# Kernel optimization log

Hardware: AMD Instinct MI355X
Metric: run time of the kernel (lower is better)

The kernel has to match this reference:

```python
import jax, jax.numpy as jnp
import numpy as np

MAX_RADIUS = 3.0
N_BASIS = 3
H = 100
C_IN = 23
N_ATOMS = 286
B = 32
Y0 = 1.0 / (2.0 * np.sqrt(np.pi))  # l=0 spherical harmonic


def cosine_basis(r):
    # e3nn CosineBasisModel basis: triangle-clamped then cosine bump
    radii = jnp.linspace(0.0, MAX_RADIUS, N_BASIS)
    step = radii[1] - radii[0]
    z = (r[..., None] - radii) / step                      # [..., N_BASIS]
    tri = 1.0 - jax.nn.relu(2.0 - jax.nn.relu(z + 1.0))    # clamp to [-1, 1]
    return jnp.cos(0.5 * jnp.pi * tri)


def setup_inputs() -> dict:
    key = jax.random.key(0)
    ks = jax.random.split(key, 10)
    def lin(k, fan_in, fan_out):
        return jax.random.normal(k, (fan_in, fan_out), jnp.float32) / np.sqrt(fan_in)
    return {
        "x": jax.random.normal(ks[0], (B, 1), jnp.float32),
        "features": jax.random.normal(ks[1], (B, N_ATOMS, C_IN), jnp.float32),
        "geometry": jax.random.normal(ks[2], (B, N_ATOMS, 3), jnp.float32),
        # radial MLP (CosineBasisModel, L=1 hidden layer of width h=100)
        "rW1": lin(ks[3], N_BASIS, H), "rb1": jnp.zeros((H,), jnp.float32),
        "rW2": lin(ks[4], H, C_IN),    "rb2": jnp.zeros((C_IN,), jnp.float32),
        # MLP head
        "fc1W": lin(ks[5], N_ATOMS, 30), "fc1b": jnp.zeros((30,), jnp.float32),
        "fc2W": lin(ks[6], 30, 10),      "fc2b": jnp.zeros((10,), jnp.float32),
        "fc3W": lin(ks[7], 10, 1),       "fc3b": jnp.zeros((1,), jnp.float32),
    }


def reference(x, features, geometry, rW1, rb1, rW2, rb2,
              fc1W, fc1b, fc2W, fc2b, fc3W, fc3b):
    Bz, N, _ = features.shape
    # pairwise distances r_ab = |geom_b - geom_a|, [B, N, N]
    diff = geometry[:, None, :, :] - geometry[:, :, None, :]
    r = jnp.sqrt(jnp.sum(diff * diff, axis=-1) + 1e-12)
    # radial kernel: cosine basis -> MLP -> 23 scalar-path weights per pair
    basis = cosine_basis(r)                                  # [B, N, N, 3]
    h = jax.nn.relu(basis @ rW1 + rb1)                       # [B, N, N, 100]
    R = (h @ rW2 + rb2) * Y0                                 # [B, N, N, 23]
    # scalar (l=0 -> l=0) point convolution, normalized by 1/sqrt(N)
    feats_new = jnp.einsum('zabj,zbj->za', R, features) * (1.0 / np.sqrt(N))
    # MLP head (fc1 consumes the [B, 286] conv output directly)
    out = jax.nn.relu(feats_new @ fc1W + fc1b)
    out = jax.nn.relu(out @ fc2W + fc2b)
    return out @ fc3W + fc3b                                 # [B, 1]
```

## Files before the change

### kernel.cpp

```cpp
#include <hip/hip_runtime.h>

#define NA      286
#define CIN     23
#define NKH     100
#define NKP     50
#define KPH     25
#define BATCH   32
#define NB_PAD  320
#define TB      64
#define ATILE   12
#define APW     3
#define NTILE_A 24
#define NTILE_B 5
#define KQ_N    5
#define KQ_SZ   10

#define Y0F      0.28209479177387814f
#define RSQRT_N  0.05913123960994873f

typedef _Float16 h2v __attribute__((ext_vector_type(2)));
union F4H { float4 f; h2v h[4]; };

__device__ __forceinline__ h2v h2_splat(float x) {
    _Float16 v = (_Float16)x;
    h2v r; r.x = v; r.y = v; return r;
}
__device__ __forceinline__ h2v h2_pack(float a, float b) {
    h2v r; r.x = (_Float16)a; r.y = (_Float16)b; return r;
}
__device__ __forceinline__ h2v h2_fma(h2v a, h2v b, h2v c) {
#if __has_builtin(__builtin_elementwise_fma)
    return __builtin_elementwise_fma(a, b, c);
#else
    return a * b + c;
#endif
}
__device__ __forceinline__ h2v h2_max0(h2v a) {
    h2v z; z.x = (_Float16)0.f; z.y = (_Float16)0.f;
#if __has_builtin(__builtin_elementwise_max)
    return __builtin_elementwise_max(a, z);
#else
    h2v r; r.x = a.x > z.x ? a.x : z.x; r.y = a.y > z.y ? a.y : z.y; return r;
#endif
}
__device__ __forceinline__ float fdot2f(h2v a, h2v b, float c) {
#if __has_builtin(__builtin_amdgcn_fdot2)
    return __builtin_amdgcn_fdot2(a, b, c, false);
#else
    return c + (float)a.x * (float)b.x + (float)a.y * (float)b.y;
#endif
}

__device__ __forceinline__ float cos_half_pi(float x) {
    float t = 1.5707963267948966f * x;
    float w = t * t;
    return 1.f + w * (-0.5f + w * (4.16666667e-2f + w * (-1.38888889e-3f
               + w * 2.48015873e-5f)));
}

__global__ void __launch_bounds__(256) prep_kernel(
    const float* __restrict__ feat,
    const float* __restrict__ rW2,
    const float* __restrict__ rW1,
    const float* __restrict__ rb1,
    h2v* __restrict__ cbuf2,
    float4* __restrict__ wpk)
{
    __shared__ float flds[TB * CIN];
    __shared__ float wlds[2 * KQ_SZ * CIN];
    const int tid = threadIdx.x;
    const int bT  = blockIdx.x;
    const int z   = blockIdx.y;
    const int kQ  = blockIdx.z;

    if (bT == 0 && z == 0 && kQ == 0 && tid < NKP) {
        int k0 = 2 * tid, k1 = k0 + 1;
        F4H u;
        u.h[0] = h2_pack(rW1[k0],           rW1[k1]);
        u.h[1] = h2_pack(rW1[NKH + k0],     rW1[NKH + k1]);
        u.h[2] = h2_pack(rW1[2 * NKH + k0], rW1[2 * NKH + k1]);
        u.h[3] = h2_pack(rb1[k0],           rb1[k1]);
        wpk[tid] = u.f;
    }

    const int b0 = bT * TB;
    const int nf = ((NA - b0 < TB) ? (NA - b0) : TB) * CIN;
    const float* fsrc = feat + ((size_t)z * NA + b0) * CIN;
    for (int i = tid; i < TB * CIN; i += 256)
        flds[i] = (i < nf) ? fsrc[i] : 0.f;
    const float* wsrc = rW2 + (size_t)kQ * KQ_SZ * 2 * CIN;
    for (int i = tid; i < 2 * KQ_SZ * CIN; i += 256)
        wlds[i] = wsrc[i];
    __syncthreads();

    for (int i = tid; i < TB * KQ_SZ; i += 256) {
        int b   = i & 63;
        int kpl = i >> 6;
        const float* w0 = &wlds[(2 * kpl) * CIN];
        const float* w1 = &wlds[(2 * kpl + 1) * CIN];
        const float* fb = &flds[b * CIN];
        float s0 = 0.f, s1 = 0.f;
#pragma unroll
        for (int j = 0; j < CIN; ++j) {
            s0 = fmaf(fb[j], w0[j], s0);
            s1 = fmaf(fb[j], w1[j], s1);
        }
        int kp = kQ * KQ_SZ + kpl;
        cbuf2[((size_t)z * NKP + kp) * NB_PAD + b0 + b] = h2_pack(s0 * Y0F, s1 * Y0F);
    }
}

__global__ void __launch_bounds__(256) pair_kernel(
    const float* __restrict__ geom,
    const h2v* __restrict__ cbuf2,
    const float4* __restrict__ wpk,
    float* __restrict__ feats_part)
{
    __shared__ float ga[ATILE * 3];

    const int tid   = threadIdx.x;
    const int z     = blockIdx.y;
    const int kh    = blockIdx.z;
    const int aBase = blockIdx.x * ATILE;

    if (tid < ATILE * 3) {
        int aa = aBase + tid / 3;
        int d  = tid - 3 * (tid / 3);
        ga[tid] = (aa < NA) ? geom[((size_t)z * NA + aa) * 3 + d] : 0.f;
    }
    __syncthreads();

    const int wave = tid >> 6;
    const int lane = tid & 63;

    float acc[APW] = {0.f, 0.f, 0.f};
    const h2v*    csrc = cbuf2 + ((size_t)z * NKP + kh * KPH) * NB_PAD;
    const float4* wsrc = wpk + kh * KPH;

    for (int t = 0; t < NTILE_B; ++t) {
        const int b = t * TB + lane;
        float gbx = 0.f, gby = 0.f, gbz = 0.f;
        if (b < NA) {
            const float* g = geom + ((size_t)z * NA + b) * 3;
            gbx = g[0]; gby = g[1]; gbz = g[2];
        }

        h2v u0[APW], u1[APW], u2[APW];
#pragma unroll
        for (int i = 0; i < APW; ++i) {
            const float* gp = &ga[(wave * APW + i) * 3];
            float dx = gbx - gp[0], dy = gby - gp[1], dz = gbz - gp[2];
            float r  = sqrtf(fmaf(dx, dx, fmaf(dy, dy, fmaf(dz, dz, 1e-12f))));
            float zz = r * (1.f / 1.5f);
            u0[i] = h2_splat(cos_half_pi(fminf(zz, 1.f)));
            u1[i] = h2_splat(cos_half_pi(fminf(fmaxf(zz - 1.f, -1.f), 1.f)));
            u2[i] = h2_splat(cos_half_pi(fminf(fmaxf(zz - 2.f, -1.f), 1.f)));
        }

        const h2v* cp = csrc + t * TB + lane;
#pragma unroll 5
        for (int kp = 0; kp < KPH; ++kp) {
            F4H u; u.f = wsrc[kp];
            h2v cb = cp[(size_t)kp * NB_PAD];
#pragma unroll
            for (int i = 0; i < APW; ++i) {
                h2v s = h2_fma(u0[i], u.h[0],
                        h2_fma(u1[i], u.h[1],
                        h2_fma(u2[i], u.h[2], u.h[3])));
                acc[i] = fdot2f(h2_max0(s), cb, acc[i]);
            }
        }
    }

#pragma unroll
    for (int i = 0; i < APW; ++i) {
        float v = acc[i];
        for (int off = 32; off; off >>= 1) v += __shfl_xor(v, off);
        if (lane == 0) {
            int a = aBase + wave * APW + i;
            if (a < NA) feats_part[((size_t)kh * BATCH + z) * 288 + a] = v * RSQRT_N;
        }
    }
}

__global__ void __launch_bounds__(256) head_kernel(
    const float* __restrict__ featsP,
    const float* __restrict__ featIn,
    const float* __restrict__ rb2,
    const float* __restrict__ fc1W, const float* __restrict__ fc1b,
    const float* __restrict__ fc2W, const float* __restrict__ fc2b,
    const float* __restrict__ fc3W, const float* __restrict__ fc3b,
    float* __restrict__ out)
{
    __shared__ float fsum[NA];
    __shared__ float ps[8][CIN];
    __shared__ float po[8][30], pw[8][30];
    __shared__ float czs;
    __shared__ float h1[30], hh2[10];

    const int z = blockIdx.x, tid = threadIdx.x;

    for (int a = tid; a < NA; a += 256)
        fsum[a] = featsP[z * 288 + a] + featsP[(BATCH + z) * 288 + a];

    if (tid < 8 * CIN) {
        int j = tid % CIN, ch = tid / CIN;
        int b0 = ch * 36, b1 = (b0 + 36 < NA) ? b0 + 36 : NA;
        float s = 0.f;
        for (int b = b0; b < b1; ++b) s += featIn[((size_t)z * NA + b) * CIN + j];
        ps[ch][j] = s;
    }
    __syncthreads();
    if (tid < CIN) {
        float s = 0.f;
#pragma unroll
        for (int ch = 0; ch < 8; ++ch) s += ps[ch][tid];
        ps[0][tid] = s * rb2[tid];
    }
    __syncthreads();
    if (tid == 0) {
        float s = 0.f;
#pragma unroll
        for (int j = 0; j < CIN; ++j) s += ps[0][j];
        czs = s * (Y0F * RSQRT_N);
    }

    if (tid < 240) {
        int j = tid % 30, ch = tid / 30;
        int a0 = ch * 36, a1 = (a0 + 36 < NA) ? a0 + 36 : NA;
        float o = 0.f, ws = 0.f;
        for (int a = a0; a < a1; ++a) {
            float w = fc1W[a * 30 + j];
            o  = fmaf(fsum[a], w, o);
            ws += w;
        }
        po[ch][j] = o; pw[ch][j] = ws;
    }
    __syncthreads();
    if (tid < 30) {
        float o = 0.f, ws = 0.f;
#pragma unroll
        for (int ch = 0; ch < 8; ++ch) { o += po[ch][tid]; ws += pw[ch][tid]; }
        h1[tid] = fmaxf(o + czs * ws + fc1b[tid], 0.f);
    }
    __syncthreads();
    if (tid < 10) {
        float v = fc2b[tid];
#pragma unroll
        for (int t = 0; t < 30; ++t) v = fmaf(h1[t], fc2W[t * 10 + tid], v);
        hh2[tid] = fmaxf(v, 0.f);
    }
    __syncthreads();
    if (tid == 0) {
        float v = fc3b[0];
#pragma unroll
        for (int t = 0; t < 10; ++t) v = fmaf(hh2[t], fc3W[t], v);
        out[z] = v;
    }
}

extern "C" void kernel_launch(void* const* d_in, const int* in_sizes, int n_in,
                              void* d_out, int out_size, void* d_ws, size_t ws_size,
                              hipStream_t stream) {
    const float* features = (const float*)d_in[1];
    const float* geometry = (const float*)d_in[2];
    const float* rW1  = (const float*)d_in[3];
    const float* rb1  = (const float*)d_in[4];
    const float* rW2  = (const float*)d_in[5];
    const float* rb2  = (const float*)d_in[6];
    const float* fc1W = (const float*)d_in[7];
    const float* fc1b = (const float*)d_in[8];
    const float* fc2W = (const float*)d_in[9];
    const float* fc2b = (const float*)d_in[10];
    const float* fc3W = (const float*)d_in[11];
    const float* fc3b = (const float*)d_in[12];

    char* ws = (char*)d_ws;
    float4* wpk    = (float4*)ws;
    h2v*    cbuf2  = (h2v*)(ws + 1024);
    float*  featsP = (float*)(ws + 1024 + (size_t)BATCH * NKP * NB_PAD * 4);

    float* out = (float*)d_out;

    prep_kernel<<<dim3(NTILE_B, BATCH, KQ_N), 256, 0, stream>>>(
        features, rW2, rW1, rb1, cbuf2, wpk);
    pair_kernel<<<dim3(NTILE_A, BATCH, 2), 256, 0, stream>>>(
        geometry, cbuf2, wpk, featsP);
    head_kernel<<<BATCH, 256, 0, stream>>>(
        featsP, features, rb2, fc1W, fc1b, fc2W, fc2b, fc3W, fc3b, out);
}
```

Baseline: 143.4 us.

## Split pair kernel over b-tiles, stage c-buffer and weights in LDS

The pair kernel's grid dimension changes from two halves of the hidden units to five b-atom tiles. Each block loads its 50x64 c-buffer slice and the packed radial weights into LDS, and computes the cosine basis once per block rather than once per tile loop iteration. The head kernel now sums five partial outputs instead of two, and a few loops get unroll pragmas. This adds parallelism and replaces global/L2 loads in the inner loop with LDS reads, at the cost of more LDS traffic and a larger partial-output buffer.

```diff
diff --git a/kernel.cpp b/kernel.cpp
--- a/kernel.cpp
+++ b/kernel.cpp
@@ -4,7 +4,6 @@
 #define CIN     23
 #define NKH     100
 #define NKP     50
-#define KPH     25
 #define BATCH   32
 #define NB_PAD  320
 #define TB      64
@@ -110,65 +109,79 @@
     }
 }
 
-__global__ void __launch_bounds__(256) pair_kernel(
+__global__ void __launch_bounds__(256, 8) pair_kernel(
     const float* __restrict__ geom,
     const h2v* __restrict__ cbuf2,
     const float4* __restrict__ wpk,
     float* __restrict__ feats_part)
 {
-    __shared__ float ga[ATILE * 3];
+    __shared__ h2v    c_lds[NKP * TB];
+    __shared__ float4 w_lds[NKP];
+    __shared__ float  ga[ATILE * 3];
 
     const int tid   = threadIdx.x;
     const int z     = blockIdx.y;
-    const int kh    = blockIdx.z;
+    const int bT    = blockIdx.z;
     const int aBase = blockIdx.x * ATILE;
 
-    if (tid < ATILE * 3) {
-        int aa = aBase + tid / 3;
-        int d  = tid - 3 * (tid / 3);
-        ga[tid] = (aa < NA) ? geom[((size_t)z * NA + aa) * 3 + d] : 0.f;
+    {
+        const uint4* s4 = (const uint4*)(cbuf2 + (size_t)z * NKP * NB_PAD + bT * TB);
+        uint4*       d4 = (uint4*)c_lds;
+#pragma unroll
+        for (int r = 0; r < 4; ++r) {
+            int i = r * 256 + tid;
+            if (i < NKP * 16) {
+                int row = i >> 4, col = i & 15;
+                d4[i] = s4[(size_t)row * (NB_PAD / 4) + col];
+            }
+        }
+    }
+    if (tid < NKP) ((uint4*)w_lds)[tid] = ((const uint4*)wpk)[tid];
+    if (tid >= 128 && tid < 128 + ATILE * 3) {
+        int t  = tid - 128;
+        int aa = aBase + t / 3;
+        int d  = t - 3 * (t / 3);
+        ga[t] = (aa < NA) ? geom[((size_t)z * NA + aa) * 3 + d] : 0.f;
     }
     __syncthreads();
 
     const int wave = tid >> 6;
     const int lane = tid & 63;
 
+    const int b = bT * TB + lane;
+    float gbx = 0.f, gby = 0.f, gbz = 0.f;
+    if (b < NA) {
+        const float* g = geom + ((size_t)z * NA + b) * 3;
+        gbx = g[0]; gby = g[1]; gbz = g[2];
+    }
+
+    h2v u0[APW], u1[APW], u2[APW];
+#pragma unroll
+    for (int i = 0; i < APW; ++i) {
+        float axv = ga[(wave * APW + i) * 3 + 0];
+        float ayv = ga[(wave * APW + i) * 3 + 1];
+        float azv = ga[(wave * APW + i) * 3 + 2];
+        float dx = gbx - axv, dy = gby - ayv, dz = gbz - azv;
+        float r  = sqrtf(fmaf(dx, dx, fmaf(dy, dy, fmaf(dz, dz, 1e-12f))));
+        float zz = r * (1.f / 1.5f);
+        u0[i] = h2_splat(cos_half_pi(fminf(zz, 1.f)));
+        u1[i] = h2_splat(cos_half_pi(fminf(fmaxf(zz - 1.f, -1.f), 1.f)));
+        u2[i] = h2_splat(cos_half_pi(fminf(fmaxf(zz - 2.f, -1.f), 1.f)));
+    }
+
     float acc[APW] = {0.f, 0.f, 0.f};
-    const h2v*    csrc = cbuf2 + ((size_t)z * NKP + kh * KPH) * NB_PAD;
-    const float4* wsrc = wpk + kh * KPH;
-
-    for (int t = 0; t < NTILE_B; ++t) {
-        const int b = t * TB + lane;
-        float gbx = 0.f, gby = 0.f, gbz = 0.f;
-        if (b < NA) {
-            const float* g = geom + ((size_t)z * NA + b) * 3;
-            gbx = g[0]; gby = g[1]; gbz = g[2];
-        }
-
-        h2v u0[APW], u1[APW], u2[APW];
+    const h2v* cl = c_lds + lane;
+
+#pragma unroll 10
+    for (int kp = 0; kp < NKP; ++kp) {
+        F4H u; u.f = w_lds[kp];
+        h2v cb = cl[kp * TB];
 #pragma unroll
         for (int i = 0; i < APW; ++i) {
-            const float* gp = &ga[(wave * APW + i) * 3];
-            float dx = gbx - gp[0], dy = gby - gp[1], dz = gbz - gp[2];
-            float r  = sqrtf(fmaf(dx, dx, fmaf(dy, dy, fmaf(dz, dz, 1e-12f))));
-            float zz = r * (1.f / 1.5f);
-            u0[i] = h2_splat(cos_half_pi(fminf(zz, 1.f)));
-            u1[i] = h2_splat(cos_half_pi(fminf(fmaxf(zz - 1.f, -1.f), 1.f)));
-            u2[i] = h2_splat(cos_half_pi(fminf(fmaxf(zz - 2.f, -1.f), 1.f)));
-        }
-
-        const h2v* cp = csrc + t * TB + lane;
-#pragma unroll 5
-        for (int kp = 0; kp < KPH; ++kp) {
-            F4H u; u.f = wsrc[kp];
-            h2v cb = cp[(size_t)kp * NB_PAD];
-#pragma unroll
-            for (int i = 0; i < APW; ++i) {
-                h2v s = h2_fma(u0[i], u.h[0],
-                        h2_fma(u1[i], u.h[1],
-                        h2_fma(u2[i], u.h[2], u.h[3])));
-                acc[i] = fdot2f(h2_max0(s), cb, acc[i]);
-            }
+            h2v s = h2_fma(u0[i], u.h[0],
+                    h2_fma(u1[i], u.h[1],
+                    h2_fma(u2[i], u.h[2], u.h[3])));
+            acc[i] = fdot2f(h2_max0(s), cb, acc[i]);
         }
     }
 
@@ -178,7 +191,8 @@
         for (int off = 32; off; off >>= 1) v += __shfl_xor(v, off);
         if (lane == 0) {
             int a = aBase + wave * APW + i;
-            if (a < NA) feats_part[((size_t)kh * BATCH + z) * 288 + a] = v * RSQRT_N;
+            if (a < NA)
+                feats_part[((size_t)bT * BATCH + z) * 288 + a] = v * RSQRT_N;
         }
     }
 }
@@ -200,13 +214,19 @@
 
     const int z = blockIdx.x, tid = threadIdx.x;
 
-    for (int a = tid; a < NA; a += 256)
-        fsum[a] = featsP[z * 288 + a] + featsP[(BATCH + z) * 288 + a];
+    for (int a = tid; a < NA; a += 256) {
+        float s = 0.f;
+#pragma unroll
+        for (int bt = 0; bt < NTILE_B; ++bt)
+            s += featsP[((size_t)bt * BATCH + z) * 288 + a];
+        fsum[a] = s;
+    }
 
     if (tid < 8 * CIN) {
         int j = tid % CIN, ch = tid / CIN;
         int b0 = ch * 36, b1 = (b0 + 36 < NA) ? b0 + 36 : NA;
         float s = 0.f;
+#pragma unroll 4
         for (int b = b0; b < b1; ++b) s += featIn[((size_t)z * NA + b) * CIN + j];
         ps[ch][j] = s;
     }
@@ -229,6 +249,7 @@
         int j = tid % 30, ch = tid / 30;
         int a0 = ch * 36, a1 = (a0 + 36 < NA) ? a0 + 36 : NA;
         float o = 0.f, ws = 0.f;
+#pragma unroll 4
         for (int a = a0; a < a1; ++a) {
             float w = fc1W[a * 30 + j];
             o  = fmaf(fsum[a], w, o);
@@ -284,7 +305,7 @@
 
     prep_kernel<<<dim3(NTILE_B, BATCH, KQ_N), 256, 0, stream>>>(
         features, rW2, rW1, rb1, cbuf2, wpk);
-    pair_kernel<<<dim3(NTILE_A, BATCH, 2), 256, 0, stream>>>(
+    pair_kernel<<<dim3(NTILE_A, BATCH, NTILE_B), 256, 0, stream>>>(
         geometry, cbuf2, wpk, featsP);
     head_kernel<<<BATCH, 256, 0, stream>>>(
         featsP, features, rb2, fc1W, fc1b, fc2W, fc2b, fc3W, fc3b, out);
```

Result: faster. 122.3 us (-14.7%).
